# Kernel optimization log

Measured on AMD Instinct MI355X. Metric: run time of the kernel, lower is better.

Reference implementation:

```python
import jax, jax.numpy as jnp
import numpy as np

WS = 4        # window_size
HEADS = 12    # num_heads


def setup_inputs() -> dict:
    key = jax.random.key(0)
    k1, k2, k3 = jax.random.split(key, 3)
    B, N, E = 32, 4096, 384
    x = jax.random.normal(k1, (B, N, E), dtype=jnp.float32)
    w_in = jax.random.normal(k2, (3 * E, E), dtype=jnp.float32) * 0.02
    b_in = jnp.zeros((3 * E,), dtype=jnp.float32)
    w_out = jax.random.normal(k3, (E, E), dtype=jnp.float32) * 0.02
    b_out = jnp.zeros((E,), dtype=jnp.float32)
    return {"x": x, "w_in": w_in, "b_in": b_in, "w_out": w_out, "b_out": b_out}


def reference(x, w_in, b_in, w_out, b_out):
    B, N, E = x.shape
    H = W = int(np.sqrt(N))
    nh, nw = H // WS, W // WS
    hd = E // HEADS
    T = WS * WS  # tokens per window

    # window partition: [B, H, W, E] -> [B*nh*nw, T, E]
    xw = x.reshape(B, nh, WS, nw, WS, E)
    xw = xw.transpose(0, 1, 3, 2, 4, 5).reshape(-1, T, E)

    # packed QKV projection (torch nn.MultiheadAttention in_proj)
    qkv = xw @ w_in.T + b_in                      # [nWin, T, 3E]
    q, k, v = jnp.split(qkv, 3, axis=-1)          # each [nWin, T, E]

    def split_heads(t):
        return t.reshape(-1, T, HEADS, hd).transpose(0, 2, 1, 3)  # [nWin, h, T, hd]

    q, k, v = split_heads(q), split_heads(k), split_heads(v)
    scale = 1.0 / np.sqrt(hd).astype(np.float32)
    scores = jnp.einsum('whqd,whkd->whqk', q * scale, k)          # [nWin, h, T, T]
    attn = jax.nn.softmax(scores, axis=-1)
    out = jnp.einsum('whqk,whkd->whqd', attn, v)                  # [nWin, h, T, hd]
    out = out.transpose(0, 2, 1, 3).reshape(-1, T, E)
    out = out @ w_out.T + b_out                                   # out_proj

    # window reverse: [B*nh*nw, T, E] -> [B, N, E]
    out = out.reshape(B, nh, nw, WS, WS, E)
    out = out.transpose(0, 1, 3, 2, 4, 5).reshape(B, N, E)
    return out
```

## Files before the change

kernel.cpp:

```cpp
#include <hip/hip_runtime.h>
#include <hip/hip_bf16.h>

typedef __attribute__((ext_vector_type(8))) short short8;
typedef __attribute__((ext_vector_type(4))) float f32x4;

static __device__ __forceinline__ f32x4 MFMA16(short8 a, short8 b, f32x4 c) {
    return __builtin_amdgcn_mfma_f32_16x16x32_bf16(a, b, c, 0, 0, 0);
}
static __device__ __forceinline__ unsigned short f2bf(float f) {
    union { __hip_bfloat16 h; unsigned short u; } c;
    c.h = __float2bfloat16(f);
    return c.u;
}
static __device__ __forceinline__ void gload16(const void* g, void* l) {
    __builtin_amdgcn_global_load_lds(
        (const __attribute__((address_space(1))) unsigned int*)g,
        (__attribute__((address_space(3))) unsigned int*)l, 16, 0, 0);
}

constexpr size_t kWstOff = 0;
constexpr size_t kWosOff = 884736;
constexpr size_t kBrrOff = 1179648;
constexpr size_t kAttOff = 1184256;

__global__ void prep(const float* __restrict__ w_in, const float* __restrict__ b_in,
                     const float* __restrict__ w_out,
                     char* __restrict__ wst, char* __restrict__ wos,
                     float* __restrict__ brr)
{
    const int i = blockIdx.x * 256 + threadIdx.x;
    if (i < 55296) {
        int hp = i / 9216, rem = i % 9216;
        int s = rem / 1536, slot16 = rem % 1536;
        int row = slot16 >> 3, sl = slot16 & 7;
        int c8 = sl ^ (row & 7);
        int hh = row / 96, rr = row % 96;
        int sec = rr >> 5, d = rr & 31;
        int srow = sec * 384 + (hp * 2 + hh) * 32 + d;
        int k0 = s * 64 + c8 * 8;
        const float4* src = (const float4*)(w_in + (size_t)srow * 384 + k0);
        float4 a = src[0], b = src[1];
        uint4 w;
        w.x = f2bf(a.x) | ((unsigned)f2bf(a.y) << 16);
        w.y = f2bf(a.z) | ((unsigned)f2bf(a.w) << 16);
        w.z = f2bf(b.x) | ((unsigned)f2bf(b.y) << 16);
        w.w = f2bf(b.z) | ((unsigned)f2bf(b.w) << 16);
        *(uint4*)(wst + (size_t)i * 16) = w;
    } else {
        int j = i - 55296;
        int nb = j / 6144, rem = j % 6144;
        int s = rem / 1024, slot16 = rem % 1024;
        int row = slot16 >> 3, sl = slot16 & 7;
        int c8 = sl ^ (row & 7);
        int srow = nb * 128 + row;
        int k0 = s * 64 + c8 * 8;
        const float4* src = (const float4*)(w_out + (size_t)srow * 384 + k0);
        float4 a = src[0], b = src[1];
        uint4 w;
        w.x = f2bf(a.x) | ((unsigned)f2bf(a.y) << 16);
        w.y = f2bf(a.z) | ((unsigned)f2bf(a.w) << 16);
        w.z = f2bf(b.x) | ((unsigned)f2bf(b.y) << 16);
        w.w = f2bf(b.z) | ((unsigned)f2bf(b.w) << 16);
        *(uint4*)(wos + (size_t)j * 16) = w;
    }
    if (i < 1152) {
        int h = i / 96, jj = i % 96;
        int sec = jj >> 5, d = jj & 31;
        brr[i] = b_in[sec * 384 + h * 32 + d];
    }
}

__global__ __launch_bounds__(256, 2)
void qkv_attn(const float* __restrict__ x, const char* __restrict__ wst,
              const float* __restrict__ brr, char* __restrict__ attst)
{
    __shared__ __align__(16) char smem[65536];

    const int tid  = threadIdx.x;
    const int lane = tid & 63, wid = tid >> 6;
    const int g = lane >> 4, r16 = lane & 15;
    const int wm = wid >> 1, wn = wid & 1;

    int b = blockIdx.x;
    int L = (b & 7) * 768 + (b >> 3);
    const int mblk = L / 6, hp = L - mblk * 6;
    const int head = hp * 2 + wn;

    const int arow = tid >> 1, ahalf = tid & 1;
    int T0 = mblk * 128 + arow;
    int win0 = T0 >> 4, t4 = T0 & 15;
    int bb0 = win0 >> 8, wh = (win0 >> 4) & 15, ww = win0 & 15;
    const float* xrow = x + ((size_t)bb0 * 4096 +
                             (size_t)((wh * 4 + (t4 >> 2)) * 64 + ww * 4 + (t4 & 3))) * 384
                          + ahalf * 32;

    float4 af[8];
    auto load_A = [&](int s) {
        const float4* xp = (const float4*)(xrow + s * 64);
        #pragma unroll
        for (int j = 0; j < 8; ++j) af[j] = xp[j];
    };
    auto write_A = [&]() {
        #pragma unroll
        for (int j = 0; j < 4; ++j) {
            uint4 w;
            w.x = f2bf(af[2*j].x)   | ((unsigned)f2bf(af[2*j].y)   << 16);
            w.y = f2bf(af[2*j].z)   | ((unsigned)f2bf(af[2*j].w)   << 16);
            w.z = f2bf(af[2*j+1].x) | ((unsigned)f2bf(af[2*j+1].y) << 16);
            w.w = f2bf(af[2*j+1].z) | ((unsigned)f2bf(af[2*j+1].w) << 16);
            int slot = (ahalf * 4 + j) ^ (arow & 7);
            *(uint4*)(smem + arow * 128 + slot * 16) = w;
        }
    };
    const char* wst_blk = wst + (size_t)hp * 147456;
    auto stage_B = [&](int s, int buf) {
        char* dst = smem + 16384 + buf * 24576 + wid * 6144;
        const char* src = wst_blk + s * 24576 + wid * 6144 + lane * 16;
        #pragma unroll
        for (int j = 0; j < 6; ++j) gload16(src + j * 1024, dst + j * 1024);
    };

    f32x4 acc[4][6] = {};
    auto compute = [&](int buf) {
        const char* bbp = smem + 16384 + buf * 24576;
        #pragma unroll
        for (int c = 0; c < 2; ++c) {
            const int sw = ((c * 4 + g) ^ (r16 & 7)) << 4;
            short8 a[4], bf[6];
            #pragma unroll
            for (int mi = 0; mi < 4; ++mi)
                a[mi] = *(const short8*)(smem + (wm * 64 + mi * 16 + r16) * 128 + sw);
            #pragma unroll
            for (int ni = 0; ni < 6; ++ni)
                bf[ni] = *(const short8*)(bbp + (wn * 96 + ni * 16 + r16) * 128 + sw);
            #pragma unroll
            for (int mi = 0; mi < 4; ++mi)
                #pragma unroll
                for (int ni = 0; ni < 6; ++ni)
                    acc[mi][ni] = MFMA16(a[mi], bf[ni], acc[mi][ni]);
        }
    };

    load_A(0);
    stage_B(0, 0);
    write_A();
    for (int s = 0; s < 6; ++s) {
        __syncthreads();
        if (s < 5) { stage_B(s + 1, (s + 1) & 1); load_A(s + 1); }
        compute(s & 1);
        __syncthreads();
        if (s < 5) write_A();
    }

    float bias[6];
    #pragma unroll
    for (int ni = 0; ni < 6; ++ni) bias[ni] = brr[head * 96 + ni * 16 + r16];

    #pragma unroll
    for (int mi = 0; mi < 4; ++mi) {
        const int win = wm * 4 + mi;
        #pragma unroll
        for (int ni = 0; ni < 6; ++ni) {
            const int sec = ni >> 1;
            const int d = (ni & 1) * 16 + r16;
            float v0 = acc[mi][ni][0] + bias[ni];
            float v1 = acc[mi][ni][1] + bias[ni];
            float v2 = acc[mi][ni][2] + bias[ni];
            float v3 = acc[mi][ni][3] + bias[ni];
            uint2 w;
            w.x = f2bf(v0) | ((unsigned)f2bf(v1) << 16);
            w.y = f2bf(v2) | ((unsigned)f2bf(v3) << 16);
            *(uint2*)(smem + win * 6144 + wn * 3072 + sec * 1024 + d * 32 + g * 8) = w;
        }
    }

    const float kC = 0.17677669529663687f * 1.4426950408889634f;
    const f32x4 zero = {0.f, 0.f, 0.f, 0.f};
    char* pt = smem + 49152 + wid * 1280;

    #pragma unroll
    for (int i = 0; i < 4; ++i) {
        const int win = wm * 4 + i;
        const char* base = smem + win * 6144 + wn * 3072;

        union U8 { unsigned short e[8]; short8 v; };
        U8 ku, qu;
        #pragma unroll
        for (int j = 0; j < 8; ++j) {
            const int off = (g * 8 + j) * 32 + r16 * 2;
            qu.e[j] = *(const unsigned short*)(base + off);
            ku.e[j] = *(const unsigned short*)(base + 1024 + off);
        }
        f32x4 s = MFMA16(ku.v, qu.v, zero);

        float m = fmaxf(fmaxf(s[0], s[1]), fmaxf(s[2], s[3]));
        m = fmaxf(m, __shfl_xor(m, 16, 64));
        m = fmaxf(m, __shfl_xor(m, 32, 64));
        float p[4], sum = 0.f;
        #pragma unroll
        for (int r = 0; r < 4; ++r) { p[r] = exp2f((s[r] - m) * kC); sum += p[r]; }
        sum += __shfl_xor(sum, 16, 64);
        sum += __shfl_xor(sum, 32, 64);
        const float inv = 1.f / sum;

        uint2 pw;
        pw.x = f2bf(p[0] * inv) | ((unsigned)f2bf(p[1] * inv) << 16);
        pw.y = f2bf(p[2] * inv) | ((unsigned)f2bf(p[3] * inv) << 16);
        *(uint2*)(pt + r16 * 80 + g * 8) = pw;

        short8 pa = *(const short8*)(pt + r16 * 80 + g * 16);
        f32x4 o[2];
        #pragma unroll
        for (int ti = 0; ti < 2; ++ti) {
            short8 vb = (short8)0;
            if (g < 2)
                vb = *(const short8*)(base + 2048 + (ti * 16 + r16) * 32 + g * 16);
            o[ti] = MFMA16(pa, vb, zero);
        }
        #pragma unroll
        for (int ti = 0; ti < 2; ++ti) {
            #pragma unroll
            for (int r = 0; r < 4; ++r) {
                int row7 = win * 16 + g * 4 + r;
                int col = head * 32 + ti * 16 + r16;
                int sst = col >> 6;
                int sl = ((col >> 3) & 7) ^ (row7 & 7);
                *(unsigned short*)(attst + (size_t)mblk * 98304 + sst * 16384
                                   + row7 * 128 + sl * 16 + (col & 7) * 2)
                    = f2bf(o[ti][r]);
            }
        }
    }
}

__global__ __launch_bounds__(256, 2)
void out_proj(const char* __restrict__ attst, const char* __restrict__ wos,
              const float* __restrict__ b_out, float* __restrict__ out)
{
    __shared__ __align__(16) char smem[65536];

    const int tid  = threadIdx.x;
    const int lane = tid & 63, wid = tid >> 6;
    const int g = lane >> 4, r16 = lane & 15;
    const int wm = wid >> 1, wn = wid & 1;

    int b = blockIdx.x;
    int L = (b & 7) * 384 + (b >> 3);
    const int mblk = L / 3, nblk = L - mblk * 3;

    auto stage = [&](int s, int buf) {
        const char* asrc = attst + (size_t)mblk * 98304 + s * 16384 + wid * 4096 + lane * 16;
        const char* bsrc = wos   + (size_t)nblk * 98304 + s * 16384 + wid * 4096 + lane * 16;
        char* adst = smem + buf * 16384 + wid * 4096;
        char* bdst = smem + 32768 + buf * 16384 + wid * 4096;
        #pragma unroll
        for (int j = 0; j < 4; ++j) {
            gload16(asrc + j * 1024, adst + j * 1024);
            gload16(bsrc + j * 1024, bdst + j * 1024);
        }
    };

    f32x4 acc[4][4] = {};
    auto compute = [&](int buf) {
        const char* ab = smem + buf * 16384;
        const char* bbp = smem + 32768 + buf * 16384;
        #pragma unroll
        for (int c = 0; c < 2; ++c) {
            const int sw = ((c * 4 + g) ^ (r16 & 7)) << 4;
            short8 a[4], bf[4];
            #pragma unroll
            for (int mi = 0; mi < 4; ++mi)
                a[mi] = *(const short8*)(ab + (wm * 64 + mi * 16 + r16) * 128 + sw);
            #pragma unroll
            for (int ni = 0; ni < 4; ++ni)
                bf[ni] = *(const short8*)(bbp + (wn * 64 + ni * 16 + r16) * 128 + sw);
            #pragma unroll
            for (int mi = 0; mi < 4; ++mi)
                #pragma unroll
                for (int ni = 0; ni < 4; ++ni)
                    acc[mi][ni] = MFMA16(a[mi], bf[ni], acc[mi][ni]);
        }
    };

    stage(0, 0);
    for (int s = 0; s < 6; ++s) {
        __syncthreads();
        if (s < 5) stage(s + 1, (s + 1) & 1);
        compute(s & 1);
    }

    float bias[4];
    #pragma unroll
    for (int ni = 0; ni < 4; ++ni) bias[ni] = b_out[nblk * 128 + wn * 64 + ni * 16 + r16];

    #pragma unroll
    for (int mi = 0; mi < 4; ++mi) {
        #pragma unroll
        for (int r = 0; r < 4; ++r) {
            int T = mblk * 128 + wm * 64 + mi * 16 + g * 4 + r;
            int win = T >> 4, tt = T & 15;
            int bb = win >> 8, wh = (win >> 4) & 15, ww = win & 15;
            size_t o = ((size_t)bb * 4096 + (wh * 4 + (tt >> 2)) * 64 + ww * 4 + (tt & 3)) * 384
                     + nblk * 128 + wn * 64;
            #pragma unroll
            for (int ni = 0; ni < 4; ++ni)
                out[o + ni * 16 + r16] = acc[mi][ni][r] + bias[ni];
        }
    }
}

extern "C" void kernel_launch(void* const* d_in, const int* in_sizes, int n_in,
                              void* d_out, int out_size, void* d_ws, size_t ws_size,
                              hipStream_t stream) {
    const float* x     = (const float*)d_in[0];
    const float* w_in  = (const float*)d_in[1];
    const float* b_in  = (const float*)d_in[2];
    const float* w_out = (const float*)d_in[3];
    const float* b_out = (const float*)d_in[4];
    float* out = (float*)d_out;

    char* ws = (char*)d_ws;
    char*  wst = ws + kWstOff;
    char*  wos = ws + kWosOff;
    float* brr = (float*)(ws + kBrrOff);
    char*  att = ws + kAttOff;

    prep<<<dim3(288), dim3(256), 0, stream>>>(w_in, b_in, w_out, wst, wos, brr);
    qkv_attn<<<dim3(6144), dim3(256), 0, stream>>>(x, wst, brr, att);
    out_proj<<<dim3(3072), dim3(256), 0, stream>>>(att, wos, b_out, out);
}
```

Baseline: 335.9 us.

## Double-buffer A tile to drop a barrier and feed P to MFMA directly

The bf16 A tile in LDS is now double-buffered, so the next stage's conversion and write can follow compute without a second __syncthreads per iteration. LDS grows from 64 KB to 80 KB per block, which may cut the two-blocks-per-CU occupancy the launch bounds ask for. The softmax probabilities now go straight from registers into the PV MFMA, using zero-padded k-slices instead of a round trip through LDS. The V operand is loaded as 8-byte chunks to match that layout.

Measured after the change: 333.8 us. Within noise of the previous version (-0.6%).

```diff
diff --git a/kernel.cpp b/kernel.cpp
--- a/kernel.cpp
+++ b/kernel.cpp
@@ -74,7 +74,7 @@
 void qkv_attn(const float* __restrict__ x, const char* __restrict__ wst,
               const float* __restrict__ brr, char* __restrict__ attst)
 {
-    __shared__ __align__(16) char smem[65536];
+    __shared__ __align__(16) char smem[81920];
 
     const int tid  = threadIdx.x;
     const int lane = tid & 63, wid = tid >> 6;
@@ -100,7 +100,7 @@
         #pragma unroll
         for (int j = 0; j < 8; ++j) af[j] = xp[j];
     };
-    auto write_A = [&]() {
+    auto write_A = [&](int buf) {
         #pragma unroll
         for (int j = 0; j < 4; ++j) {
             uint4 w;
@@ -109,12 +109,12 @@
             w.z = f2bf(af[2*j+1].x) | ((unsigned)f2bf(af[2*j+1].y) << 16);
             w.w = f2bf(af[2*j+1].z) | ((unsigned)f2bf(af[2*j+1].w) << 16);
             int slot = (ahalf * 4 + j) ^ (arow & 7);
-            *(uint4*)(smem + arow * 128 + slot * 16) = w;
+            *(uint4*)(smem + buf * 16384 + arow * 128 + slot * 16) = w;
         }
     };
     const char* wst_blk = wst + (size_t)hp * 147456;
     auto stage_B = [&](int s, int buf) {
-        char* dst = smem + 16384 + buf * 24576 + wid * 6144;
+        char* dst = smem + 32768 + buf * 24576 + wid * 6144;
         const char* src = wst_blk + s * 24576 + wid * 6144 + lane * 16;
         #pragma unroll
         for (int j = 0; j < 6; ++j) gload16(src + j * 1024, dst + j * 1024);
@@ -122,14 +122,15 @@
 
     f32x4 acc[4][6] = {};
     auto compute = [&](int buf) {
-        const char* bbp = smem + 16384 + buf * 24576;
+        const char* ab = smem + buf * 16384;
+        const char* bbp = smem + 32768 + buf * 24576;
         #pragma unroll
         for (int c = 0; c < 2; ++c) {
             const int sw = ((c * 4 + g) ^ (r16 & 7)) << 4;
             short8 a[4], bf[6];
             #pragma unroll
             for (int mi = 0; mi < 4; ++mi)
-                a[mi] = *(const short8*)(smem + (wm * 64 + mi * 16 + r16) * 128 + sw);
+                a[mi] = *(const short8*)(ab + (wm * 64 + mi * 16 + r16) * 128 + sw);
             #pragma unroll
             for (int ni = 0; ni < 6; ++ni)
                 bf[ni] = *(const short8*)(bbp + (wn * 96 + ni * 16 + r16) * 128 + sw);
@@ -143,14 +144,14 @@
 
     load_A(0);
     stage_B(0, 0);
-    write_A();
+    write_A(0);
     for (int s = 0; s < 6; ++s) {
         __syncthreads();
-        if (s < 5) { stage_B(s + 1, (s + 1) & 1); load_A(s + 1); }
+        if (s < 5) { load_A(s + 1); stage_B(s + 1, (s + 1) & 1); }
         compute(s & 1);
-        __syncthreads();
-        if (s < 5) write_A();
-    }
+        if (s < 5) write_A((s + 1) & 1);
+    }
+    __syncthreads();
 
     float bias[6];
     #pragma unroll
@@ -176,7 +177,6 @@
 
     const float kC = 0.17677669529663687f * 1.4426950408889634f;
     const f32x4 zero = {0.f, 0.f, 0.f, 0.f};
-    char* pt = smem + 49152 + wid * 1280;
 
     #pragma unroll
     for (int i = 0; i < 4; ++i) {
@@ -203,19 +203,18 @@
         sum += __shfl_xor(sum, 32, 64);
         const float inv = 1.f / sum;
 
-        uint2 pw;
-        pw.x = f2bf(p[0] * inv) | ((unsigned)f2bf(p[1] * inv) << 16);
-        pw.y = f2bf(p[2] * inv) | ((unsigned)f2bf(p[3] * inv) << 16);
-        *(uint2*)(pt + r16 * 80 + g * 8) = pw;
-
-        short8 pa = *(const short8*)(pt + r16 * 80 + g * 16);
+        U8 pu;
+        pu.e[0] = f2bf(p[0] * inv); pu.e[1] = f2bf(p[1] * inv);
+        pu.e[2] = f2bf(p[2] * inv); pu.e[3] = f2bf(p[3] * inv);
+        pu.e[4] = 0; pu.e[5] = 0; pu.e[6] = 0; pu.e[7] = 0;
+
         f32x4 o[2];
         #pragma unroll
         for (int ti = 0; ti < 2; ++ti) {
-            short8 vb = (short8)0;
-            if (g < 2)
-                vb = *(const short8*)(base + 2048 + (ti * 16 + r16) * 32 + g * 16);
-            o[ti] = MFMA16(pa, vb, zero);
+            U8 vu;
+            *(uint2*)&vu.e[0] = *(const uint2*)(base + 2048 + (ti * 16 + r16) * 32 + g * 8);
+            vu.e[4] = 0; vu.e[5] = 0; vu.e[6] = 0; vu.e[7] = 0;
+            o[ti] = MFMA16(pu.v, vu.v, zero);
         }
         #pragma unroll
         for (int ti = 0; ti < 2; ++ti) {
```
